# Performance work log

Hardware: AMD Instinct MI355X
Metric: run time of the kernel (lower is better)

The kernel has to match this reference:

```python
import jax, jax.numpy as jnp
import numpy as np

B, K, D, NH = 4096, 32, 1024, 16
HD = D // NH
LN_EPS = 1e-5
RMS_EPS = 1e-6


def layernorm(x, g, b):
    mu = jnp.mean(x, axis=-1, keepdims=True)
    var = jnp.mean((x - mu) ** 2, axis=-1, keepdims=True)
    return (x - mu) * jax.lax.rsqrt(var + LN_EPS) * g + b


def rmsnorm(x, g):
    ms = jnp.mean(x ** 2, axis=-1, keepdims=True)
    return x * jax.lax.rsqrt(ms + RMS_EPS) * g


def setup_inputs() -> dict:
    key = jax.random.key(0)
    ks = jax.random.split(key, 12)
    s = 0.02
    inp = {
        "query": jax.random.normal(ks[0], (B, D), jnp.float32),
        "point_features": jax.random.normal(ks[1], (B, K, D), jnp.float32),
        "lnq_g": jnp.ones((D,), jnp.float32),
        "lnq_b": jnp.zeros((D,), jnp.float32),
        "lnkv_g": jnp.ones((D,), jnp.float32),
        "lnkv_b": jnp.zeros((D,), jnp.float32),
        "Wq": jax.random.normal(ks[2], (D, D), jnp.float32) * s,
        "bq": jnp.zeros((D,), jnp.float32),
        "Wk": jax.random.normal(ks[3], (D, D), jnp.float32) * s,
        "bk": jnp.zeros((D,), jnp.float32),
        "Wv": jax.random.normal(ks[4], (D, D), jnp.float32) * s,
        "bv": jnp.zeros((D,), jnp.float32),
        "rmsq_g": jnp.ones((D,), jnp.float32),
        "rmsk_g": jnp.ones((D,), jnp.float32),
        "Wo": jax.random.normal(ks[5], (D, D), jnp.float32) * s,
        "bo": jnp.zeros((D,), jnp.float32),
        "mlpn_g": jnp.ones((D,), jnp.float32),
        "mlpn_b": jnp.zeros((D,), jnp.float32),
        "W1": jax.random.normal(ks[6], (D, 4 * D), jnp.float32) * s,
        "b1": jnp.zeros((4 * D,), jnp.float32),
        "W2": jax.random.normal(ks[7], (4 * D, D), jnp.float32) * s,
        "b2": jnp.zeros((D,), jnp.float32),
    }
    return inp


def reference(query, point_features, lnq_g, lnq_b, lnkv_g, lnkv_b,
              Wq, bq, Wk, bk, Wv, bv, rmsq_g, rmsk_g, Wo, bo,
              mlpn_g, mlpn_b, W1, b1, W2, b2):
    q_in = layernorm(query, lnq_g, lnq_b)            # [B, D]
    kv_in = layernorm(point_features, lnkv_g, lnkv_b)  # [B, K, D]

    q = rmsnorm(q_in @ Wq + bq, rmsq_g)              # [B, D]
    k = rmsnorm(kv_in @ Wk + bk, rmsk_g)             # [B, K, D]
    v = kv_in @ Wv + bv                               # [B, K, D]

    # Faithful to original: raw row-major reshape [B,K,D] -> [B,NH,K,HD]
    qh = q.reshape(B, NH, HD)                         # [B, NH, HD] (q_len = 1)
    kh = k.reshape(B, NH, K, HD)
    vh = v.reshape(B, NH, K, HD)

    scores = jnp.einsum('bhd,bhkd->bhk', qh, kh) / np.sqrt(HD).astype(np.float32)
    attn = jax.nn.softmax(scores, axis=-1)            # [B, NH, K]
    out = jnp.einsum('bhk,bhkd->bhd', attn, vh)       # [B, NH, HD]

    # Faithful: transpose(1,2) then reshape -> [B, HD, NH] -> [B, D]
    out = jnp.transpose(out, (0, 2, 1)).reshape(B, D)
    out = (out @ Wo + bo) + query                     # residual

    h = layernorm(out, mlpn_g, mlpn_b)
    mlp_out = (jax.nn.gelu(h @ W1 + b1, approximate=False) @ W2) + b2
    return out + mlp_out
```

## Files before the change

### kernel.cpp

```cpp
#include <hip/hip_runtime.h>
#include <stdint.h>

#define DEVI __device__ __forceinline__

typedef unsigned short u16;
typedef short s8v __attribute__((ext_vector_type(8)));
typedef float f4v __attribute__((ext_vector_type(4)));
typedef u16 u16x4 __attribute__((ext_vector_type(4)));

DEVI u16 f2bf(float f) {
  unsigned u = __float_as_uint(f);
  u += 0x7fffu + ((u >> 16) & 1u);
  return (u16)(u >> 16);
}
DEVI float bf2f(u16 h) { return __uint_as_float(((unsigned)h) << 16); }

DEVI void gload16(const void* g, void* l) {
  __builtin_amdgcn_global_load_lds(
      (const __attribute__((address_space(1))) void*)(uintptr_t)g,
      (__attribute__((address_space(3))) void*)(uintptr_t)l, 16, 0, 0);
}

__global__ __launch_bounds__(256) void transpose_w(const float* __restrict__ W,
                                                   u16* __restrict__ Wt, int R, int C) {
  __shared__ float tile[32][33];
  const int tx = threadIdx.x & 31, ty = threadIdx.x >> 5;
  const int r0 = blockIdx.y * 32, c0 = blockIdx.x * 32;
#pragma unroll
  for (int i = 0; i < 4; ++i)
    tile[ty + 8 * i][tx] = W[(size_t)(r0 + ty + 8 * i) * C + c0 + tx];
  __syncthreads();
#pragma unroll
  for (int i = 0; i < 4; ++i)
    Wt[(size_t)(c0 + ty + 8 * i) * R + r0 + tx] = f2bf(tile[tx][ty + 8 * i]);
}

__global__ __launch_bounds__(256) void ln_rows(const float* __restrict__ x,
                                               const float* __restrict__ g,
                                               const float* __restrict__ bsh,
                                               u16* __restrict__ y,
                                               float* __restrict__ zbuf) {
  const size_t row = blockIdx.x;
  const int t = threadIdx.x;
  if (zbuf && t == 0) zbuf[row] = 0.f;
  float4 v = ((const float4*)(x + row * 1024))[t];
  float s = v.x + v.y + v.z + v.w;
  float q = v.x * v.x + v.y * v.y + v.z * v.z + v.w * v.w;
#pragma unroll
  for (int m = 1; m < 64; m <<= 1) { s += __shfl_xor(s, m); q += __shfl_xor(q, m); }
  __shared__ float sh[8];
  if ((t & 63) == 0) { sh[t >> 6] = s; sh[4 + (t >> 6)] = q; }
  __syncthreads();
  s = sh[0] + sh[1] + sh[2] + sh[3];
  q = sh[4] + sh[5] + sh[6] + sh[7];
  const float mu = s * (1.f / 1024.f);
  const float var = q * (1.f / 1024.f) - mu * mu;
  const float rs = rsqrtf(var + 1e-5f);
  const int c = t * 4;
  const float in[4] = {v.x, v.y, v.z, v.w};
  u16x4 o;
#pragma unroll
  for (int i = 0; i < 4; ++i) o[i] = f2bf((in[i] - mu) * rs * g[c + i] + bsh[c + i]);
  *(u16x4*)(y + row * 1024 + c) = o;
}

template <int EPI>
__global__ __launch_bounds__(512, 2) void gemm256(
    const u16* __restrict__ A, const u16* __restrict__ Bt,
    const float* __restrict__ biasK, const float* __restrict__ biasV,
    const float* __restrict__ gcol, u16* __restrict__ CK, u16* __restrict__ CV,
    float* __restrict__ rowssq, int M, int N, int K, int RB, int CB) {
  __shared__ u16 lds[4][16384];
  const int t = threadIdx.x;
  const int lane = t & 63;
  const int wave = t >> 6;
  const int wm = wave >> 2, wn = wave & 3;
  const int fr = lane & 15, kq = lane >> 4;

  const int bid = blockIdx.x;
  const int cpx = gridDim.x >> 3;
  const int swz = (bid & 7) * cpx + (bid >> 3);
  const int rb = swz / CB, cb = swz % CB;
  const size_t row0 = (size_t)rb * 256, col0 = (size_t)cb * 256;

  f4v acc[8][4];
#pragma unroll
  for (int i = 0; i < 8; ++i)
#pragma unroll
    for (int n = 0; n < 4; ++n) acc[i][n] = (f4v){0.f, 0.f, 0.f, 0.f};

  const int srow = t >> 2;
  const int scol = (((t & 3) ^ ((t >> 3) & 3)) << 3);
  const u16* Ag0 = A + (row0 + srow) * (size_t)K + scol;
  const u16* Ag1 = Ag0 + (size_t)128 * K;
  const u16* Bg0 = Bt + (col0 + srow) * (size_t)K + scol;
  const u16* Bg1 = Bg0 + (size_t)128 * K;

  const int kx = ((kq ^ ((fr >> 1) & 3)) << 3);

  const int NT = K >> 5;

#pragma unroll
  for (int tt = 0; tt < 3; ++tt) {
    u16* sA = &lds[tt][0];
    u16* sB = &lds[tt][8192];
    gload16(Ag0 + tt * 32, sA + t * 8);
    gload16(Ag1 + tt * 32, sA + 4096 + t * 8);
    gload16(Bg0 + tt * 32, sB + t * 8);
    gload16(Bg1 + tt * 32, sB + 4096 + t * 8);
  }

#pragma unroll 4
  for (int T = 0; T < NT; ++T) {
    asm volatile("s_waitcnt vmcnt(8)" ::: "memory");
    __builtin_amdgcn_s_barrier();
    __builtin_amdgcn_sched_barrier(0);
    const u16* sA = &lds[T & 3][0];
    const u16* sB = &lds[T & 3][8192];
    const int Ts = (T + 3 < NT) ? T + 3 : NT - 1;
    u16* dA = &lds[(T + 3) & 3][0];
    u16* dB = &lds[(T + 3) & 3][8192];
    s8v a[4], b[4];
#pragma unroll
    for (int m = 0; m < 4; ++m)
      a[m] = *(const s8v*)&sA[(wm * 128 + m * 16 + fr) * 32 + kx];
#pragma unroll
    for (int n = 0; n < 4; ++n)
      b[n] = *(const s8v*)&sB[(wn * 64 + n * 16 + fr) * 32 + kx];
    gload16(Ag0 + Ts * 32, dA + t * 8);
    gload16(Ag1 + Ts * 32, dA + 4096 + t * 8);
    __builtin_amdgcn_s_barrier();
    asm volatile("s_waitcnt lgkmcnt(0)" ::: "memory");
    __builtin_amdgcn_sched_barrier(0);
    __builtin_amdgcn_s_setprio(1);
#pragma unroll
    for (int m = 0; m < 4; ++m)
#pragma unroll
      for (int n = 0; n < 4; ++n)
        acc[m][n] = __builtin_amdgcn_mfma_f32_16x16x32_bf16(a[m], b[n], acc[m][n], 0, 0, 0);
    __builtin_amdgcn_s_setprio(0);
    __builtin_amdgcn_s_barrier();
#pragma unroll
    for (int m = 0; m < 4; ++m)
      a[m] = *(const s8v*)&sA[(wm * 128 + 64 + m * 16 + fr) * 32 + kx];
    gload16(Bg0 + Ts * 32, dB + t * 8);
    gload16(Bg1 + Ts * 32, dB + 4096 + t * 8);
    __builtin_amdgcn_s_barrier();
    asm volatile("s_waitcnt lgkmcnt(0)" ::: "memory");
    __builtin_amdgcn_sched_barrier(0);
    __builtin_amdgcn_s_setprio(1);
#pragma unroll
    for (int m = 0; m < 4; ++m)
#pragma unroll
      for (int n = 0; n < 4; ++n)
        acc[4 + m][n] = __builtin_amdgcn_mfma_f32_16x16x32_bf16(a[m], b[n], acc[4 + m][n], 0, 0, 0);
    __builtin_amdgcn_s_setprio(0);
  }

  const int kq4 = kq * 4;
  if (EPI == 0) {
    const bool isK = (col0 < 1024);
    if (isK) {
#pragma unroll
      for (int ai = 0; ai < 8; ++ai) {
        int cols[4];
        float bb[4], gg[4];
#pragma unroll
        for (int n = 0; n < 4; ++n) {
          cols[n] = (int)col0 + wn * 64 + n * 16 + fr;
          bb[n] = biasK[cols[n]];
          gg[n] = gcol[cols[n]];
        }
#pragma unroll
        for (int r = 0; r < 4; ++r) {
          const size_t grow = row0 + wm * 128 + ai * 16 + kq4 + r;
          float v[4];
#pragma unroll
          for (int n = 0; n < 4; ++n) v[n] = acc[ai][n][r] + bb[n];
          float s = v[0] * v[0] + v[1] * v[1] + v[2] * v[2] + v[3] * v[3];
          s += __shfl_xor(s, 1);
          s += __shfl_xor(s, 2);
          s += __shfl_xor(s, 4);
          s += __shfl_xor(s, 8);
          if (fr == 0) atomicAdd(&rowssq[grow], s);
#pragma unroll
          for (int n = 0; n < 4; ++n)
            CK[grow * 1024 + cols[n]] = f2bf(v[n] * gg[n]);
        }
      }
    } else {
#pragma unroll
      for (int ai = 0; ai < 8; ++ai) {
        int cols[4];
        float bb[4];
#pragma unroll
        for (int n = 0; n < 4; ++n) {
          cols[n] = (int)col0 - 1024 + wn * 64 + n * 16 + fr;
          bb[n] = biasV[cols[n]];
        }
#pragma unroll
        for (int r = 0; r < 4; ++r) {
          const size_t grow = row0 + wm * 128 + ai * 16 + kq4 + r;
#pragma unroll
          for (int n = 0; n < 4; ++n)
            CV[grow * 1024 + cols[n]] = f2bf(acc[ai][n][r] + bb[n]);
        }
      }
    }
  } else {
#pragma unroll
    for (int ai = 0; ai < 8; ++ai) {
      int cols[4];
      float bb[4];
#pragma unroll
      for (int n = 0; n < 4; ++n) {
        cols[n] = (int)col0 + wn * 64 + n * 16 + fr;
        bb[n] = biasK[cols[n]];
      }
#pragma unroll
      for (int r = 0; r < 4; ++r) {
        const size_t grow = row0 + wm * 128 + ai * 16 + kq4 + r;
#pragma unroll
        for (int n = 0; n < 4; ++n) {
          const float x = acc[ai][n][r] + bb[n];
          CK[grow * (size_t)N + cols[n]] = f2bf(0.5f * x * (1.f + erff(x * 0.70710678118654752f)));
        }
      }
    }
  }
}

template <int EPI>
__global__ __launch_bounds__(256) void gemm_bt(
    const u16* __restrict__ A, const u16* __restrict__ Bt,
    const float* __restrict__ bias, const float* __restrict__ gcol,
    void* __restrict__ Cv, const float* __restrict__ extra,
    float* __restrict__ rowssq, int M, int N, int K) {
  __shared__ u16 As[128 * 32];
  __shared__ u16 Bs[128 * 32];
  const int t = threadIdx.x;
  const int lane = t & 63;
  const int wave = t >> 6;
  const int wr = wave >> 1, wc = wave & 1;
  const size_t row0 = (size_t)blockIdx.y * 128;
  const size_t col0 = (size_t)blockIdx.x * 128;
  int Ksub = K, koff = 0;
  if (EPI == 6) { Ksub = K / gridDim.z; koff = blockIdx.z * Ksub; }

  f4v acc[4][4];
#pragma unroll
  for (int m = 0; m < 4; ++m)
#pragma unroll
    for (int n = 0; n < 4; ++n) acc[m][n] = (f4v){0.f, 0.f, 0.f, 0.f};

  const int sr = t >> 2;
  const int scw = (((t & 3) ^ ((t >> 3) & 3)) << 3);
  const u16* Ag = A + (row0 + sr) * (size_t)K + koff + scw;
  const u16* Bg = Bt + (col0 + sr) * (size_t)K + koff + scw;
  u16* Al = &As[t * 8];
  u16* Bl = &Bs[t * 8];
  const int fr = lane & 15;
  const int kx = (((lane >> 4) ^ ((fr >> 1) & 3)) << 3);

  for (int k0 = 0; k0 < Ksub; k0 += 32) {
    gload16(Ag + k0, Al);
    gload16(Ag + k0 + (size_t)64 * K, Al + 64 * 32);
    gload16(Bg + k0, Bl);
    gload16(Bg + k0 + (size_t)64 * K, Bl + 64 * 32);
    __syncthreads();
    s8v a[4], b[4];
#pragma unroll
    for (int m = 0; m < 4; ++m)
      a[m] = *(const s8v*)&As[(wr * 64 + m * 16 + fr) * 32 + kx];
#pragma unroll
    for (int n = 0; n < 4; ++n)
      b[n] = *(const s8v*)&Bs[(wc * 64 + n * 16 + fr) * 32 + kx];
#pragma unroll
    for (int m = 0; m < 4; ++m)
#pragma unroll
      for (int n = 0; n < 4; ++n)
        acc[m][n] = __builtin_amdgcn_mfma_f32_16x16x32_bf16(a[m], b[n], acc[m][n], 0, 0, 0);
    __syncthreads();
  }

  float* Cp = (float*)Cv;
  if (EPI == 6) Cp += (size_t)blockIdx.z * M * (size_t)N;
  const int rg = (lane >> 4) * 4;
#pragma unroll
  for (int m = 0; m < 4; ++m) {
    int cols[4];
    float bvals[4];
#pragma unroll
    for (int n = 0; n < 4; ++n) {
      cols[n] = (int)col0 + wc * 64 + n * 16 + fr;
      bvals[n] = (EPI == 6) ? 0.f : bias[cols[n]];
    }
#pragma unroll
    for (int r = 0; r < 4; ++r) {
      const size_t grow = row0 + wr * 64 + m * 16 + rg + r;
      float v[4];
#pragma unroll
      for (int n = 0; n < 4; ++n) v[n] = acc[m][n][r] + bvals[n];
      if (EPI == 5) {
        float s = v[0] * v[0] + v[1] * v[1] + v[2] * v[2] + v[3] * v[3];
        s += __shfl_xor(s, 1);
        s += __shfl_xor(s, 2);
        s += __shfl_xor(s, 4);
        s += __shfl_xor(s, 8);
        if (fr == 0) atomicAdd(&rowssq[grow], s);
      }
#pragma unroll
      for (int n = 0; n < 4; ++n) {
        const size_t idx = grow * (size_t)N + cols[n];
        if (EPI == 3) {
          Cp[idx] = v[n] + extra[idx];
        } else if (EPI == 5) {
          ((u16*)Cv)[idx] = f2bf(v[n]);
        } else if (EPI == 6) {
          Cp[idx] = v[n];
        }
      }
    }
  }
}

__global__ __launch_bounds__(256) void attn_k(const u16* __restrict__ qf,
                                              const u16* __restrict__ kmat,
                                              const float* __restrict__ kssq,
                                              const u16* __restrict__ vmat,
                                              const float* __restrict__ gq,
                                              const float* __restrict__ qssq,
                                              u16* __restrict__ ao) {
  const int lb = blockIdx.x;
  const int t = threadIdx.x;
  const int wave = t >> 6, lane = t & 63;
  const int j = lane & 31, half = lane >> 5;
  const float rq = rsqrtf(qssq[lb] * (1.f / 1024.f) + 1e-6f) * 0.125f;
  __shared__ float po[64][17];
#pragma unroll
  for (int hi = 0; hi < 4; ++hi) {
    const int h = wave * 4 + hi;
    const int krow = lb * 32 + 2 * h + (j >> 4);
    const u16* kp = kmat + (size_t)krow * 1024 + (j & 15) * 64 + half * 32;
    const u16* qp = qf + (size_t)lb * 1024 + h * 64 + half * 32;
    const float* gqp = gq + h * 64 + half * 32;
    float s = 0.f;
#pragma unroll
    for (int cc = 0; cc < 4; ++cc) {
      s8v qv = *(const s8v*)(qp + cc * 8);
      s8v kv = *(const s8v*)(kp + cc * 8);
#pragma unroll
      for (int e = 0; e < 8; ++e)
        s += bf2f((u16)qv[e]) * gqp[cc * 8 + e] * bf2f((u16)kv[e]);
    }
    s += __shfl_xor(s, 32);
    s *= rsqrtf(kssq[krow] * (1.f / 1024.f) + 1e-6f) * rq;
    float mx = s;
#pragma unroll
    for (int m = 16; m >= 1; m >>= 1) mx = fmaxf(mx, __shfl_xor(mx, m));
    const float pe = __expf(s - mx);
    float sum = pe;
#pragma unroll
    for (int m = 16; m >= 1; m >>= 1) sum += __shfl_xor(sum, m);
    const float pr = pe / sum;
    float o = 0.f;
#pragma unroll
    for (int jj = 0; jj < 32; ++jj) {
      const int vrow = lb * 32 + 2 * h + (jj >> 4);
      const float vv = bf2f(vmat[(size_t)vrow * 1024 + (jj & 15) * 64 + lane]);
      o += __shfl(pr, jj) * vv;
    }
    po[lane][h] = o;
  }
  __syncthreads();
  const int c = t * 4;
  u16x4 o4;
#pragma unroll
  for (int i = 0; i < 4; ++i) o4[i] = f2bf(po[(c + i) >> 4][(c + i) & 15]);
  *(u16x4*)(ao + (size_t)lb * 1024 + c) = o4;
}

__global__ __launch_bounds__(256) void combine_k(const float* __restrict__ p0,
                                                 const float* __restrict__ p1,
                                                 const float* __restrict__ b2,
                                                 const float* __restrict__ resid,
                                                 float* __restrict__ out) {
  const int i = blockIdx.x * 256 + threadIdx.x;
  float4 a = ((const float4*)p0)[i];
  float4 b = ((const float4*)p1)[i];
  float4 r = ((const float4*)resid)[i];
  float4 bb = ((const float4*)b2)[i & 255];
  float4 o;
  o.x = a.x + b.x + r.x + bb.x;
  o.y = a.y + b.y + r.y + bb.y;
  o.z = a.z + b.z + r.z + bb.z;
  o.w = a.w + b.w + r.w + bb.w;
  ((float4*)out)[i] = o;
}

extern "C" void kernel_launch(void* const* d_in, const int* in_sizes, int n_in,
                              void* d_out, int out_size, void* d_ws, size_t ws_size,
                              hipStream_t stream) {
  const float* query  = (const float*)d_in[0];
  const float* pf     = (const float*)d_in[1];
  const float* lnq_g  = (const float*)d_in[2];
  const float* lnq_b  = (const float*)d_in[3];
  const float* lnkv_g = (const float*)d_in[4];
  const float* lnkv_b = (const float*)d_in[5];
  const float* Wq     = (const float*)d_in[6];
  const float* bq     = (const float*)d_in[7];
  const float* Wk     = (const float*)d_in[8];
  const float* bk     = (const float*)d_in[9];
  const float* Wv     = (const float*)d_in[10];
  const float* bv     = (const float*)d_in[11];
  const float* rmsq_g = (const float*)d_in[12];
  const float* rmsk_g = (const float*)d_in[13];
  const float* Wo     = (const float*)d_in[14];
  const float* bo     = (const float*)d_in[15];
  const float* mlpn_g = (const float*)d_in[16];
  const float* mlpn_b = (const float*)d_in[17];
  const float* W1     = (const float*)d_in[18];
  const float* b1     = (const float*)d_in[19];
  const float* W2     = (const float*)d_in[20];
  const float* b2     = (const float*)d_in[21];
  float* out = (float*)d_out;

  char* p = (char*)d_ws;
  auto alloc = [&](size_t n) {
    char* r = p;
    p += (n + 255) & ~(size_t)255;
    return r;
  };

  u16* Wqt = (u16*)alloc((size_t)1024 * 1024 * 2);
  u16* KVt = (u16*)alloc((size_t)2048 * 1024 * 2);
  u16* Wot = (u16*)alloc((size_t)1024 * 1024 * 2);
  u16* W1t = (u16*)alloc((size_t)1024 * 4096 * 2);
  u16* W2t = (u16*)alloc((size_t)4096 * 1024 * 2);
  u16* qln = (u16*)alloc((size_t)4096 * 1024 * 2);
  u16* qpre = (u16*)alloc((size_t)4096 * 1024 * 2);
  float* qssq = (float*)alloc((size_t)4096 * 4);
  u16* attn_o = (u16*)alloc((size_t)4096 * 1024 * 2);
  float* outbuf = (float*)alloc((size_t)4096 * 1024 * 4);
  u16* hbuf = (u16*)alloc((size_t)4096 * 1024 * 2);
  u16* mid = (u16*)alloc((size_t)4096 * 4096 * 2);
  float* w2p = (float*)alloc((size_t)2 * 4096 * 1024 * 4);

  const size_t used = (size_t)(p - (char*)d_ws);
  int NC = 4;
  while (NC < 64) {
    size_t rows_try = (size_t)131072 / NC;
    if (used + 3 * (rows_try * 2048 + 256) + rows_try * 4 + 256 <= ws_size) break;
    NC *= 2;
  }
  const size_t rows = (size_t)131072 / NC;
  u16* kvln = (u16*)alloc(rows * 2048);
  u16* kmat = (u16*)alloc(rows * 2048);
  u16* vmat = (u16*)alloc(rows * 2048);
  float* kssq = (float*)alloc(rows * 4);

  transpose_w<<<dim3(32, 32), 256, 0, stream>>>(Wq, Wqt, 1024, 1024);
  transpose_w<<<dim3(32, 32), 256, 0, stream>>>(Wk, KVt, 1024, 1024);
  transpose_w<<<dim3(32, 32), 256, 0, stream>>>(Wv, KVt + (size_t)1024 * 1024, 1024, 1024);
  transpose_w<<<dim3(32, 32), 256, 0, stream>>>(Wo, Wot, 1024, 1024);
  transpose_w<<<dim3(128, 32), 256, 0, stream>>>(W1, W1t, 1024, 4096);
  transpose_w<<<dim3(32, 128), 256, 0, stream>>>(W2, W2t, 4096, 1024);

  ln_rows<<<4096, 256, 0, stream>>>(query, lnq_g, lnq_b, qln, qssq);
  gemm_bt<5><<<dim3(8, 32), 256, 0, stream>>>(qln, Wqt, bq, nullptr, qpre, nullptr,
                                              qssq, 4096, 1024, 1024);

  const int bpc = 4096 / NC;
  const int RB = (int)(rows / 256);
  for (int c = 0; c < NC; ++c) {
    ln_rows<<<(unsigned)rows, 256, 0, stream>>>(pf + (size_t)c * rows * 1024, lnkv_g,
                                                lnkv_b, kvln, kssq);
    gemm256<0><<<RB * 8, 512, 0, stream>>>(kvln, KVt, bk, bv, rmsk_g, kmat, vmat,
                                           kssq, (int)rows, 2048, 1024, RB, 8);
    attn_k<<<bpc, 256, 0, stream>>>(qpre + (size_t)c * bpc * 1024, kmat, kssq, vmat,
                                    rmsq_g, qssq + (size_t)c * bpc,
                                    attn_o + (size_t)c * bpc * 1024);
  }

  gemm_bt<3><<<dim3(8, 32), 256, 0, stream>>>(attn_o, Wot, bo, nullptr, outbuf, query,
                                              nullptr, 4096, 1024, 1024);
  ln_rows<<<4096, 256, 0, stream>>>(outbuf, mlpn_g, mlpn_b, hbuf, nullptr);
  gemm256<1><<<16 * 16, 512, 0, stream>>>(hbuf, W1t, b1, nullptr, nullptr, mid, nullptr,
                                          nullptr, 4096, 4096, 1024, 16, 16);
  gemm_bt<6><<<dim3(8, 32, 2), 256, 0, stream>>>(mid, W2t, nullptr, nullptr, w2p,
                                                 nullptr, nullptr, 4096, 1024, 4096);
  combine_k<<<4096, 256, 0, stream>>>(w2p, w2p + (size_t)4096 * 1024, b2, outbuf, out);
}
```

Baseline: 1.079 ms.

## Restructure gemm256 main loop into single-barrier stage with compile-time K

Makes the GEMM K dimension a template constant and precomputes per-stage LDS byte pointers, which removes per-iteration address arithmetic. Each iteration now loads all A and B fragments at once, issues all four async global-to-LDS prefetches together, and runs 32 MFMAs back to back. This drops the two extra barriers and explicit lgkmcnt waits that previously split the iteration into two halves. The trade-offs are higher register pressure from holding a0/a1/b at once, and the removed clamp on the prefetch index, so the last stages read up to 96 elements past each row.

```diff
diff --git a/kernel.cpp b/kernel.cpp
--- a/kernel.cpp
+++ b/kernel.cpp
@@ -64,12 +64,12 @@
   *(u16x4*)(y + row * 1024 + c) = o;
 }
 
-template <int EPI>
+template <int EPI, int KK>
 __global__ __launch_bounds__(512, 2) void gemm256(
     const u16* __restrict__ A, const u16* __restrict__ Bt,
     const float* __restrict__ biasK, const float* __restrict__ biasV,
     const float* __restrict__ gcol, u16* __restrict__ CK, u16* __restrict__ CV,
-    float* __restrict__ rowssq, int M, int N, int K, int RB, int CB) {
+    float* __restrict__ rowssq, int M, int N, int RB, int CB) {
   __shared__ u16 lds[4][16384];
   const int t = threadIdx.x;
   const int lane = t & 63;
@@ -91,69 +91,65 @@
 
   const int srow = t >> 2;
   const int scol = (((t & 3) ^ ((t >> 3) & 3)) << 3);
-  const u16* Ag0 = A + (row0 + srow) * (size_t)K + scol;
-  const u16* Ag1 = Ag0 + (size_t)128 * K;
-  const u16* Bg0 = Bt + (col0 + srow) * (size_t)K + scol;
-  const u16* Bg1 = Bg0 + (size_t)128 * K;
-
-  const int kx = ((kq ^ ((fr >> 1) & 3)) << 3);
-
-  const int NT = K >> 5;
+  const u16* Ag0 = A + (row0 + srow) * (size_t)KK + scol;
+  const u16* Ag1 = Ag0 + (size_t)128 * KK;
+  const u16* Bg0 = Bt + (col0 + srow) * (size_t)KK + scol;
+  const u16* Bg1 = Bg0 + (size_t)128 * KK;
+
+  const int kxb = ((kq ^ ((fr >> 1) & 3)) << 4);
+  const char* lbase = (const char*)&lds[0][0];
+  const char* bA[4];
+  const char* bB[4];
+  char* dst0[4];
+#pragma unroll
+  for (int s = 0; s < 4; ++s) {
+    bA[s] = lbase + s * 32768 + wm * 8192 + fr * 64 + kxb;
+    bB[s] = lbase + s * 32768 + 16384 + wn * 4096 + fr * 64 + kxb;
+    dst0[s] = (char*)lbase + s * 32768 + t * 16;
+  }
 
 #pragma unroll
   for (int tt = 0; tt < 3; ++tt) {
-    u16* sA = &lds[tt][0];
-    u16* sB = &lds[tt][8192];
-    gload16(Ag0 + tt * 32, sA + t * 8);
-    gload16(Ag1 + tt * 32, sA + 4096 + t * 8);
-    gload16(Bg0 + tt * 32, sB + t * 8);
-    gload16(Bg1 + tt * 32, sB + 4096 + t * 8);
-  }
-
+    gload16(Ag0 + tt * 32, dst0[tt]);
+    gload16(Ag1 + tt * 32, dst0[tt] + 8192);
+    gload16(Bg0 + tt * 32, dst0[tt] + 16384);
+    gload16(Bg1 + tt * 32, dst0[tt] + 24576);
+  }
+
+  const int NT = KK >> 5;
 #pragma unroll 4
   for (int T = 0; T < NT; ++T) {
     asm volatile("s_waitcnt vmcnt(8)" ::: "memory");
     __builtin_amdgcn_s_barrier();
     __builtin_amdgcn_sched_barrier(0);
-    const u16* sA = &lds[T & 3][0];
-    const u16* sB = &lds[T & 3][8192];
-    const int Ts = (T + 3 < NT) ? T + 3 : NT - 1;
-    u16* dA = &lds[(T + 3) & 3][0];
-    u16* dB = &lds[(T + 3) & 3][8192];
-    s8v a[4], b[4];
+    const char* sA = bA[T & 3];
+    const char* sB = bB[T & 3];
+    s8v a0[4], a1[4], b[4];
+#pragma unroll
+    for (int m = 0; m < 4; ++m) {
+      a0[m] = *(const s8v*)(sA + m * 1024);
+      a1[m] = *(const s8v*)(sA + 4096 + m * 1024);
+    }
+#pragma unroll
+    for (int n = 0; n < 4; ++n) b[n] = *(const s8v*)(sB + n * 1024);
+    {
+      char* d = dst0[(T + 3) & 3];
+      gload16(Ag0 + (T + 3) * 32, d);
+      gload16(Ag1 + (T + 3) * 32, d + 8192);
+      gload16(Bg0 + (T + 3) * 32, d + 16384);
+      gload16(Bg1 + (T + 3) * 32, d + 24576);
+    }
+    __builtin_amdgcn_s_setprio(1);
 #pragma unroll
     for (int m = 0; m < 4; ++m)
-      a[m] = *(const s8v*)&sA[(wm * 128 + m * 16 + fr) * 32 + kx];
-#pragma unroll
-    for (int n = 0; n < 4; ++n)
-      b[n] = *(const s8v*)&sB[(wn * 64 + n * 16 + fr) * 32 + kx];
-    gload16(Ag0 + Ts * 32, dA + t * 8);
-    gload16(Ag1 + Ts * 32, dA + 4096 + t * 8);
-    __builtin_amdgcn_s_barrier();
-    asm volatile("s_waitcnt lgkmcnt(0)" ::: "memory");
-    __builtin_amdgcn_sched_barrier(0);
-    __builtin_amdgcn_s_setprio(1);
+#pragma unroll
+      for (int n = 0; n < 4; ++n)
+        acc[m][n] = __builtin_amdgcn_mfma_f32_16x16x32_bf16(a0[m], b[n], acc[m][n], 0, 0, 0);
 #pragma unroll
     for (int m = 0; m < 4; ++m)
 #pragma unroll
       for (int n = 0; n < 4; ++n)
-        acc[m][n] = __builtin_amdgcn_mfma_f32_16x16x32_bf16(a[m], b[n], acc[m][n], 0, 0, 0);
-    __builtin_amdgcn_s_setprio(0);
-    __builtin_amdgcn_s_barrier();
-#pragma unroll
-    for (int m = 0; m < 4; ++m)
-      a[m] = *(const s8v*)&sA[(wm * 128 + 64 + m * 16 + fr) * 32 + kx];
-    gload16(Bg0 + Ts * 32, dB + t * 8);
-    gload16(Bg1 + Ts * 32, dB + 4096 + t * 8);
-    __builtin_amdgcn_s_barrier();
-    asm volatile("s_waitcnt lgkmcnt(0)" ::: "memory");
-    __builtin_amdgcn_sched_barrier(0);
-    __builtin_amdgcn_s_setprio(1);
-#pragma unroll
-    for (int m = 0; m < 4; ++m)
-#pragma unroll
-      for (int n = 0; n < 4; ++n)
-        acc[4 + m][n] = __builtin_amdgcn_mfma_f32_16x16x32_bf16(a[m], b[n], acc[4 + m][n], 0, 0, 0);
+        acc[4 + m][n] = __builtin_amdgcn_mfma_f32_16x16x32_bf16(a1[m], b[n], acc[4 + m][n], 0, 0, 0);
     __builtin_amdgcn_s_setprio(0);
   }
 
@@ -475,8 +471,8 @@
   for (int c = 0; c < NC; ++c) {
     ln_rows<<<(unsigned)rows, 256, 0, stream>>>(pf + (size_t)c * rows * 1024, lnkv_g,
                                                 lnkv_b, kvln, kssq);
-    gemm256<0><<<RB * 8, 512, 0, stream>>>(kvln, KVt, bk, bv, rmsk_g, kmat, vmat,
-                                           kssq, (int)rows, 2048, 1024, RB, 8);
+    gemm256<0, 1024><<<RB * 8, 512, 0, stream>>>(kvln, KVt, bk, bv, rmsk_g, kmat, vmat,
+                                                 kssq, (int)rows, 2048, RB, 8);
     attn_k<<<bpc, 256, 0, stream>>>(qpre + (size_t)c * bpc * 1024, kmat, kssq, vmat,
                                     rmsq_g, qssq + (size_t)c * bpc,
                                     attn_o + (size_t)c * bpc * 1024);
@@ -485,8 +481,8 @@
   gemm_bt<3><<<dim3(8, 32), 256, 0, stream>>>(attn_o, Wot, bo, nullptr, outbuf, query,
                                               nullptr, 4096, 1024, 1024);
   ln_rows<<<4096, 256, 0, stream>>>(outbuf, mlpn_g, mlpn_b, hbuf, nullptr);
-  gemm256<1><<<16 * 16, 512, 0, stream>>>(hbuf, W1t, b1, nullptr, nullptr, mid, nullptr,
-                                          nullptr, 4096, 4096, 1024, 16, 16);
+  gemm256<1, 1024><<<16 * 16, 512, 0, stream>>>(hbuf, W1t, b1, nullptr, nullptr, mid,
+                                                nullptr, nullptr, 4096, 4096, 16, 16);
   gemm_bt<6><<<dim3(8, 32, 2), 256, 0, stream>>>(mid, W2t, nullptr, nullptr, w2p,
                                                  nullptr, nullptr, 4096, 1024, 4096);
   combine_k<<<4096, 256, 0, stream>>>(w2p, w2p + (size_t)4096 * 1024, b2, outbuf, out);
```

After: 1.070 ms. Within noise of the previous version (-0.8%).
